# Performance work log

Measured on AMD Instinct MI355X. Metric: run time of the kernel, lower is better.

The kernel has to match this reference:

```python
import jax, jax.numpy as jnp
import numpy as np

B, T, S, R, D, F = 256, 8, 200, 8, 64, 20


def setup_inputs() -> dict:
    key = jax.random.key(0)
    ks = jax.random.split(key, 8)
    # 0.1 scale keeps attention logits in a reasonable range (like trained embeddings)
    seq = 0.1 * jax.random.normal(ks[0], (B, S, D), dtype=jnp.float32)
    delta_t_n = jax.random.uniform(ks[1], (B, S), dtype=jnp.float32)  # normalized time gaps
    target = 0.1 * jax.random.normal(ks[2], (B, T, D), dtype=jnp.float32)
    target_value = 0.1 * jax.random.normal(ks[3], (B, T, R, D), dtype=jnp.float32)
    valid_mask = jax.random.randint(ks[4], (B, 1, S, 1), 0, 2, dtype=jnp.int32)
    rel_emb = 0.1 * jax.random.normal(ks[5], (R, D), dtype=jnp.float32)
    freq_real = 0.1 * jax.random.normal(ks[6], (R, F), dtype=jnp.float32)
    freq_imag = 0.1 * jax.random.normal(ks[7], (R, F), dtype=jnp.float32)
    return dict(seq=seq, delta_t_n=delta_t_n, target=target, target_value=target_value,
                valid_mask=valid_mask, rel_emb=rel_emb, freq_real=freq_real, freq_imag=freq_imag)


def _idft_decay(delta_t_n, freq_real, freq_imag):
    # freqs: concat(linspace(0,1,F)/2, -linspace(0,1,F)/2) -> [2F]
    f = jnp.linspace(0.0, 1.0, F, dtype=jnp.float32) / 2.0
    freqs = jnp.concatenate([f, -f])
    x_real = jnp.concatenate([freq_real, freq_real], axis=-1)   # [R,2F]
    x_imag = jnp.concatenate([freq_imag, -freq_imag], axis=-1)  # [R,2F]
    w = 2.0 * jnp.pi * freqs * delta_t_n[..., None]             # [B,S,2F]
    # [B,S,1,2F] * [1,1,R,2F] -> mean over 2F -> [B,S,R]
    decay = (jnp.cos(w)[:, :, None, :] * x_real[None, None]
             - jnp.sin(w)[:, :, None, :] * x_imag[None, None]).mean(axis=-1) / 2.0
    return decay


def reference(seq, delta_t_n, target, target_value, valid_mask, rel_emb, freq_real, freq_imag):
    # include_val=True branch
    rv = rel_emb[None, None] + target_value              # [B,T,R,D]
    ri = rv * target[:, :, None, :]                      # [B,T,R,D]
    # scores: contraction over D, no [B,T,S,R,D] materialization
    att = jnp.einsum('bsd,btrd->btsr', seq, ri)          # [B,T,S,R]
    att = att - att.max()
    att = jnp.where(valid_mask == 0, -jnp.inf, att)
    att = jax.nn.softmax(att, axis=-2)                   # softmax over seq (S)
    decay = jnp.clip(_idft_decay(delta_t_n, freq_real, freq_imag), 0.0, 1.0)[:, None]  # [B,1,S,R]
    decay = jnp.where(valid_mask == 0, 0.0, decay)
    att = att * decay
    context = jnp.einsum('bsd,btsr->btrd', seq, att)     # [B,T,R,D]
    return context
```

## Files before the change

kernel.cpp:

```cpp
#include <hip/hip_runtime.h>
#include <math.h>

constexpr int kB = 256, kT = 8, kS = 200, kR = 8, kD = 64, kF = 20;

__global__ __launch_bounds__(256) void rda_fused(
    const float* __restrict__ seq,
    const float* __restrict__ dt,
    const float* __restrict__ target,
    const float* __restrict__ tv,
    const int*   __restrict__ vm,
    const float* __restrict__ rel,
    const float* __restrict__ fr,
    const float* __restrict__ fi,
    float* __restrict__ out)
{
    __shared__ float ri[kR * kD];
    __shared__ float att[kR][kS];
    __shared__ float u[2240];

    const int o = blockIdx.x;
    const int b = o & 255, t = o >> 8;
    const int bt = b * kT + t;
    const int tid = threadIdx.x, wave = tid >> 6, lane = tid & 63;

    float* dec = u;
    float* frT = u + 1600;
    float* fiT = u + 1760;
    float* part = u;

    if (tid < 2 * kR * kF) {
        int idx = tid;
        int tab = idx >= kR * kF; int j = idx - tab * kR * kF;
        u[1600 + idx] = (tab ? fi : fr)[(j & 7) * kF + (j >> 3)];
    }
    if (tid < 2 * kR * kF - 256) {
        int idx = tid + 256;
        int j = idx - kR * kF;
        u[1600 + idx] = fi[(j & 7) * kF + (j >> 3)];
    }
    {
        const float* tvb = tv + (size_t)bt * kR * kD;
        const float* tgb = target + (size_t)bt * kD;
        for (int idx = tid; idx < kR * kD; idx += 256)
            ri[idx] = (rel[idx] + tvb[idx]) * tgb[idx & 63];
    }
    __syncthreads();

    if (tid < kS) {
        const int s = tid;
        const bool valid = vm[b * kS + s] != 0;

        {
            const float tt = dt[b * kS + s];
            float acc[kR];
#pragma unroll
            for (int r = 0; r < kR; ++r) acc[r] = 0.f;
#pragma unroll
            for (int k = 0; k < kF; ++k) {
                float w = 6.283185307179586f * ((float)k * (0.5f / (kF - 1))) * tt;
                float sn, cs; __sincosf(w, &sn, &cs);
                float4 f0 = *(const float4*)&frT[k * 8];
                float4 f1 = *(const float4*)&frT[k * 8 + 4];
                float4 g0 = *(const float4*)&fiT[k * 8];
                float4 g1 = *(const float4*)&fiT[k * 8 + 4];
                acc[0] += cs * f0.x - sn * g0.x;  acc[1] += cs * f0.y - sn * g0.y;
                acc[2] += cs * f0.z - sn * g0.z;  acc[3] += cs * f0.w - sn * g0.w;
                acc[4] += cs * f1.x - sn * g1.x;  acc[5] += cs * f1.y - sn * g1.y;
                acc[6] += cs * f1.z - sn * g1.z;  acc[7] += cs * f1.w - sn * g1.w;
            }
#pragma unroll
            for (int r = 0; r < kR; ++r) {
                float v = fminf(fmaxf(acc[r] * (1.0f / (2.0f * kF)), 0.f), 1.f);
                dec[r * kS + s] = valid ? v : 0.f;
            }
        }

        {
            const float4* seqrow = (const float4*)(seq + (size_t)(b * kS + s) * kD);
            float a[kR];
#pragma unroll
            for (int r = 0; r < kR; ++r) a[r] = 0.f;
#pragma unroll
            for (int uu = 0; uu < kD / 4; ++uu) {
                float4 sv = seqrow[uu];
#pragma unroll
                for (int r = 0; r < kR; ++r) {
                    float4 rv = ((const float4*)(ri + r * kD))[uu];
                    a[r] += sv.x * rv.x + sv.y * rv.y + sv.z * rv.z + sv.w * rv.w;
                }
            }
#pragma unroll
            for (int r = 0; r < kR; ++r)
                att[r][s] = valid ? a[r] : -INFINITY;
        }
    }
    __syncthreads();

#pragma unroll
    for (int h = 0; h < 2; ++h) {
        const int r = 2 * wave + h;
        float* row = &att[r][0];
        float a0 = row[lane];
        float a1 = row[lane + 64];
        float a2 = row[lane + 128];
        float a3 = (lane < kS - 192) ? row[lane + 192] : -INFINITY;
        float m = fmaxf(fmaxf(a0, a1), fmaxf(a2, a3));
#pragma unroll
        for (int off = 32; off; off >>= 1) m = fmaxf(m, __shfl_xor(m, off));
        float e0 = __expf(a0 - m), e1 = __expf(a1 - m), e2 = __expf(a2 - m);
        float e3 = (lane < kS - 192) ? __expf(a3 - m) : 0.f;
        float ssum = e0 + e1 + e2 + e3;
#pragma unroll
        for (int off = 32; off; off >>= 1) ssum += __shfl_xor(ssum, off);
        const float inv = 1.0f / ssum;
        row[lane]       = e0 * inv * dec[r * kS + lane];
        row[lane + 64]  = e1 * inv * dec[r * kS + lane + 64];
        row[lane + 128] = e2 * inv * dec[r * kS + lane + 128];
        if (lane < kS - 192)
            row[lane + 192] = e3 * inv * dec[r * kS + lane + 192];
    }
    __syncthreads();

    {
        float acc[kR];
#pragma unroll
        for (int r = 0; r < kR; ++r) acc[r] = 0.f;
        const float* seqb = seq + (size_t)b * kS * kD + lane;
        for (int g = wave; g < kS / 4; g += 4) {
            const int s0 = 4 * g;
            float4 av[kR];
#pragma unroll
            for (int r = 0; r < kR; ++r)
                av[r] = *(const float4*)&att[r][s0];
            float sv0 = seqb[(size_t)(s0 + 0) * kD];
            float sv1 = seqb[(size_t)(s0 + 1) * kD];
            float sv2 = seqb[(size_t)(s0 + 2) * kD];
            float sv3 = seqb[(size_t)(s0 + 3) * kD];
#pragma unroll
            for (int r = 0; r < kR; ++r)
                acc[r] += sv0 * av[r].x + sv1 * av[r].y + sv2 * av[r].z + sv3 * av[r].w;
        }
#pragma unroll
        for (int r = 0; r < kR; ++r)
            part[(wave * kR + r) * kD + lane] = acc[r];
    }
    __syncthreads();

    {
        int idx = tid;
#pragma unroll
        for (int it = 0; it < 2; ++it, idx += 256) {
            float v = part[idx] + part[512 + idx] + part[1024 + idx] + part[1536 + idx];
            out[(size_t)bt * kR * kD + idx] = v;
        }
    }
}

extern "C" void kernel_launch(void* const* d_in, const int* in_sizes, int n_in,
                              void* d_out, int out_size, void* d_ws, size_t ws_size,
                              hipStream_t stream) {
    const float* seq    = (const float*)d_in[0];
    const float* dt     = (const float*)d_in[1];
    const float* target = (const float*)d_in[2];
    const float* tv     = (const float*)d_in[3];
    const int*   vm     = (const int*)  d_in[4];
    const float* rel    = (const float*)d_in[5];
    const float* fr     = (const float*)d_in[6];
    const float* fi     = (const float*)d_in[7];
    float* out = (float*)d_out;

    rda_fused<<<kB * kT, 256, 0, stream>>>(seq, dt, target, tv, vm, rel, fr, fi, out);
}
```

Before: 105.9 us.

## Hoist decay into separate per-batch kernel and reduce context via readlane broadcast

The decay computation, which depends only on batch and not on the target index, moves to its own kernel launched once per batch and written to workspace, instead of being recomputed in each of the eight target blocks. Inside that kernel the sin/cos terms come from an angle-addition recurrence seeded by a single sincos. The main kernel keeps softmax weights in registers and, per wave, accumulates two relation rows over all sequence positions using readlane broadcasts, which drops the shared-memory partial sums and two barriers. The costs are an extra kernel launch plus a global round trip for the decay table, serial per-wave loops over all 200 positions, and possible rounding drift from the recurrence.

```diff
diff --git a/kernel.cpp b/kernel.cpp
--- a/kernel.cpp
+++ b/kernel.cpp
@@ -3,41 +3,73 @@
 
 constexpr int kB = 256, kT = 8, kS = 200, kR = 8, kD = 64, kF = 20;
 
-__global__ __launch_bounds__(256) void rda_fused(
+constexpr float kW1 = 3.14159265358979323846f / 19.0f;
+
+__global__ __launch_bounds__(256) void decay_kernel(
+    const float* __restrict__ dt,
+    const float* __restrict__ fr,
+    const float* __restrict__ fi,
+    const int*   __restrict__ vm,
+    float* __restrict__ dec)
+{
+    const int b = blockIdx.x;
+    const int tid = threadIdx.x;
+    const int r = tid >> 5, j = tid & 31;
+
+    float frr[kF], fir[kF];
+    {
+        const float4* f4 = (const float4*)(fr + r * kF);
+        const float4* g4 = (const float4*)(fi + r * kF);
+#pragma unroll
+        for (int c = 0; c < 5; ++c) {
+            float4 a = f4[c], g = g4[c];
+            frr[4 * c + 0] = a.x; frr[4 * c + 1] = a.y;
+            frr[4 * c + 2] = a.z; frr[4 * c + 3] = a.w;
+            fir[4 * c + 0] = g.x; fir[4 * c + 1] = g.y;
+            fir[4 * c + 2] = g.z; fir[4 * c + 3] = g.w;
+        }
+    }
+
+#pragma unroll
+    for (int it = 0; it < 7; ++it) {
+        const int s = j + 32 * it;
+        if (s < kS) {
+            const float tt = dt[b * kS + s];
+            const bool valid = vm[b * kS + s] != 0;
+            float s1, c1;
+            __sincosf(kW1 * tt, &s1, &c1);
+            float ck = c1, sk = s1;
+            float acc = frr[0] + c1 * frr[1] - s1 * fir[1];
+#pragma unroll
+            for (int k = 2; k < kF; ++k) {
+                float cn = ck * c1 - sk * s1;
+                float sn = sk * c1 + ck * s1;
+                ck = cn; sk = sn;
+                acc += ck * frr[k] - sk * fir[k];
+            }
+            float v = fminf(fmaxf(acc * (1.0f / (2.0f * kF)), 0.f), 1.f);
+            dec[(b * kR + r) * kS + s] = valid ? v : 0.f;
+        }
+    }
+}
+
+__global__ __launch_bounds__(256) void rda_main(
     const float* __restrict__ seq,
-    const float* __restrict__ dt,
     const float* __restrict__ target,
     const float* __restrict__ tv,
     const int*   __restrict__ vm,
     const float* __restrict__ rel,
-    const float* __restrict__ fr,
-    const float* __restrict__ fi,
+    const float* __restrict__ dec,
     float* __restrict__ out)
 {
     __shared__ float ri[kR * kD];
     __shared__ float att[kR][kS];
-    __shared__ float u[2240];
 
     const int o = blockIdx.x;
     const int b = o & 255, t = o >> 8;
     const int bt = b * kT + t;
     const int tid = threadIdx.x, wave = tid >> 6, lane = tid & 63;
 
-    float* dec = u;
-    float* frT = u + 1600;
-    float* fiT = u + 1760;
-    float* part = u;
-
-    if (tid < 2 * kR * kF) {
-        int idx = tid;
-        int tab = idx >= kR * kF; int j = idx - tab * kR * kF;
-        u[1600 + idx] = (tab ? fi : fr)[(j & 7) * kF + (j >> 3)];
-    }
-    if (tid < 2 * kR * kF - 256) {
-        int idx = tid + 256;
-        int j = idx - kR * kF;
-        u[1600 + idx] = fi[(j & 7) * kF + (j >> 3)];
-    }
     {
         const float* tvb = tv + (size_t)bt * kR * kD;
         const float* tgb = target + (size_t)bt * kD;
@@ -49,57 +81,30 @@
     if (tid < kS) {
         const int s = tid;
         const bool valid = vm[b * kS + s] != 0;
-
-        {
-            const float tt = dt[b * kS + s];
-            float acc[kR];
+        const float4* seqrow = (const float4*)(seq + (size_t)(b * kS + s) * kD);
+        float a[kR];
 #pragma unroll
-            for (int r = 0; r < kR; ++r) acc[r] = 0.f;
+        for (int r = 0; r < kR; ++r) a[r] = 0.f;
 #pragma unroll
-            for (int k = 0; k < kF; ++k) {
-                float w = 6.283185307179586f * ((float)k * (0.5f / (kF - 1))) * tt;
-                float sn, cs; __sincosf(w, &sn, &cs);
-                float4 f0 = *(const float4*)&frT[k * 8];
-                float4 f1 = *(const float4*)&frT[k * 8 + 4];
-                float4 g0 = *(const float4*)&fiT[k * 8];
-                float4 g1 = *(const float4*)&fiT[k * 8 + 4];
-                acc[0] += cs * f0.x - sn * g0.x;  acc[1] += cs * f0.y - sn * g0.y;
-                acc[2] += cs * f0.z - sn * g0.z;  acc[3] += cs * f0.w - sn * g0.w;
-                acc[4] += cs * f1.x - sn * g1.x;  acc[5] += cs * f1.y - sn * g1.y;
-                acc[6] += cs * f1.z - sn * g1.z;  acc[7] += cs * f1.w - sn * g1.w;
-            }
+        for (int uu = 0; uu < kD / 4; ++uu) {
+            float4 sv = seqrow[uu];
 #pragma unroll
             for (int r = 0; r < kR; ++r) {
-                float v = fminf(fmaxf(acc[r] * (1.0f / (2.0f * kF)), 0.f), 1.f);
-                dec[r * kS + s] = valid ? v : 0.f;
+                float4 rv = ((const float4*)(ri + r * kD))[uu];
+                a[r] += sv.x * rv.x + sv.y * rv.y + sv.z * rv.z + sv.w * rv.w;
             }
         }
-
-        {
-            const float4* seqrow = (const float4*)(seq + (size_t)(b * kS + s) * kD);
-            float a[kR];
 #pragma unroll
-            for (int r = 0; r < kR; ++r) a[r] = 0.f;
-#pragma unroll
-            for (int uu = 0; uu < kD / 4; ++uu) {
-                float4 sv = seqrow[uu];
-#pragma unroll
-                for (int r = 0; r < kR; ++r) {
-                    float4 rv = ((const float4*)(ri + r * kD))[uu];
-                    a[r] += sv.x * rv.x + sv.y * rv.y + sv.z * rv.z + sv.w * rv.w;
-                }
-            }
-#pragma unroll
-            for (int r = 0; r < kR; ++r)
-                att[r][s] = valid ? a[r] : -INFINITY;
-        }
+        for (int r = 0; r < kR; ++r)
+            att[r][s] = valid ? a[r] : -INFINITY;
     }
     __syncthreads();
 
+    float pa[2][4];
 #pragma unroll
     for (int h = 0; h < 2; ++h) {
         const int r = 2 * wave + h;
-        float* row = &att[r][0];
+        const float* row = &att[r][0];
         float a0 = row[lane];
         float a1 = row[lane + 64];
         float a2 = row[lane + 128];
@@ -113,46 +118,29 @@
 #pragma unroll
         for (int off = 32; off; off >>= 1) ssum += __shfl_xor(ssum, off);
         const float inv = 1.0f / ssum;
-        row[lane]       = e0 * inv * dec[r * kS + lane];
-        row[lane + 64]  = e1 * inv * dec[r * kS + lane + 64];
-        row[lane + 128] = e2 * inv * dec[r * kS + lane + 128];
-        if (lane < kS - 192)
-            row[lane + 192] = e3 * inv * dec[r * kS + lane + 192];
+        const float* dg = dec + ((size_t)b * kR + r) * kS;
+        pa[h][0] = e0 * inv * dg[lane];
+        pa[h][1] = e1 * inv * dg[lane + 64];
+        pa[h][2] = e2 * inv * dg[lane + 128];
+        pa[h][3] = (lane < kS - 192) ? e3 * inv * dg[lane + 192] : 0.f;
     }
-    __syncthreads();
 
     {
-        float acc[kR];
+        float acc0 = 0.f, acc1 = 0.f;
+        const float* sq = seq + (size_t)b * kS * kD + lane;
 #pragma unroll
-        for (int r = 0; r < kR; ++r) acc[r] = 0.f;
-        const float* seqb = seq + (size_t)b * kS * kD + lane;
-        for (int g = wave; g < kS / 4; g += 4) {
-            const int s0 = 4 * g;
-            float4 av[kR];
-#pragma unroll
-            for (int r = 0; r < kR; ++r)
-                av[r] = *(const float4*)&att[r][s0];
-            float sv0 = seqb[(size_t)(s0 + 0) * kD];
-            float sv1 = seqb[(size_t)(s0 + 1) * kD];
-            float sv2 = seqb[(size_t)(s0 + 2) * kD];
-            float sv3 = seqb[(size_t)(s0 + 3) * kD];
-#pragma unroll
-            for (int r = 0; r < kR; ++r)
-                acc[r] += sv0 * av[r].x + sv1 * av[r].y + sv2 * av[r].z + sv3 * av[r].w;
+        for (int s = 0; s < kS; ++s) {
+            float sv = sq[(size_t)s * kD];
+            float a0 = __int_as_float(
+                __builtin_amdgcn_readlane(__float_as_int(pa[0][s >> 6]), s & 63));
+            float a1 = __int_as_float(
+                __builtin_amdgcn_readlane(__float_as_int(pa[1][s >> 6]), s & 63));
+            acc0 += sv * a0;
+            acc1 += sv * a1;
         }
-#pragma unroll
-        for (int r = 0; r < kR; ++r)
-            part[(wave * kR + r) * kD + lane] = acc[r];
-    }
-    __syncthreads();
-
-    {
-        int idx = tid;
-#pragma unroll
-        for (int it = 0; it < 2; ++it, idx += 256) {
-            float v = part[idx] + part[512 + idx] + part[1024 + idx] + part[1536 + idx];
-            out[(size_t)bt * kR * kD + idx] = v;
-        }
+        float* ob = out + (size_t)bt * kR * kD;
+        ob[(2 * wave + 0) * kD + lane] = acc0;
+        ob[(2 * wave + 1) * kD + lane] = acc1;
     }
 }
 
@@ -168,6 +156,8 @@
     const float* fr     = (const float*)d_in[6];
     const float* fi     = (const float*)d_in[7];
     float* out = (float*)d_out;
+    float* dec = (float*)d_ws;
 
-    rda_fused<<<kB * kT, 256, 0, stream>>>(seq, dt, target, tv, vm, rel, fr, fi, out);
+    decay_kernel<<<kB, 256, 0, stream>>>(dt, fr, fi, vm, dec);
+    rda_main<<<kB * kT, 256, 0, stream>>>(seq, target, tv, vm, rel, dec, out);
 }
```

New measurement: 108.3 us. 1.02x slower.
